# Kernel tuning notes

Hardware: AMD Instinct MI355X
Metric: run time of the kernel (lower is better)

The kernel has to match this reference:

```python
import jax, jax.numpy as jnp
import numpy as np

EPS = 1e-5

def layer_norm(x, w, b):
    mu = x.mean(-1, keepdims=True)
    var = x.var(-1, keepdims=True)
    return (x - mu) / jnp.sqrt(var + EPS) * w + b

def s5_forward(u, Lambda_re, Lambda_im, B_re, B_im, C_re, C_im, D, log_step):
    # u: [B, L, H]; diagonal S5 SSM with P complex states, ZOH discretization.
    Lam = (Lambda_re + 1j * Lambda_im).astype(jnp.complex64)          # [P]
    dt = jnp.exp(log_step).astype(jnp.complex64)                       # [P]
    Lam_bar = jnp.exp(Lam * dt)                                        # [P]
    Bc = (B_re + 1j * B_im).astype(jnp.complex64)                      # [P, H]
    B_bar = ((Lam_bar - 1.0) / Lam)[:, None] * Bc                      # [P, H]
    Bu = jnp.einsum('blh,ph->blp', u.astype(jnp.complex64), B_bar)     # [B, L, P]
    A = jnp.broadcast_to(Lam_bar, Bu.shape)                            # [B, L, P]

    def binop(e1, e2):
        a1, b1 = e1
        a2, b2 = e2
        return (a2 * a1, a2 * b1 + b2)

    _, xs = jax.lax.associative_scan(binop, (A, Bu), axis=1)           # [B, L, P]
    Cc = (C_re + 1j * C_im).astype(jnp.complex64)                      # [H, P]
    y = 2.0 * jnp.einsum('blp,hp->blh', xs, Cc).real + D * u           # [B, L, H]
    return y

def setup_inputs() -> dict:
    key = jax.random.key(0)
    ks = jax.random.split(key, 12)
    B, L, H, P = 4, 4096, 512, 512
    x = jax.random.normal(ks[0], (B, L, H), jnp.float32)
    # SSM params (HiPPO-like flavor: negative real part, spread imaginary part)
    Lambda_re = -(0.5 * jax.random.uniform(ks[1], (P,), jnp.float32) + 0.1)
    Lambda_im = jnp.pi * jnp.arange(P, dtype=jnp.float32)
    B_re = jax.random.normal(ks[2], (P, H), jnp.float32) / np.sqrt(2.0 * H)
    B_im = jax.random.normal(ks[3], (P, H), jnp.float32) / np.sqrt(2.0 * H)
    C_re = jax.random.normal(ks[4], (H, P), jnp.float32) / np.sqrt(P)
    C_im = jax.random.normal(ks[5], (H, P), jnp.float32) / np.sqrt(P)
    D = jax.random.normal(ks[6], (H,), jnp.float32)
    log_step = jax.random.uniform(ks[7], (P,), jnp.float32,
                                  minval=np.log(1e-3), maxval=np.log(1e-1))
    ln1_w = jnp.ones((H,), jnp.float32); ln1_b = jnp.zeros((H,), jnp.float32)
    ln2_w = jnp.ones((H,), jnp.float32); ln2_b = jnp.zeros((H,), jnp.float32)
    W_enc = jax.random.normal(ks[8], (2 * H, H), jnp.float32) / np.sqrt(H)
    W_dec = jax.random.normal(ks[9], (H, H), jnp.float32) / np.sqrt(H)
    return {"x": x, "ln1_w": ln1_w, "ln1_b": ln1_b,
            "Lambda_re": Lambda_re, "Lambda_im": Lambda_im,
            "B_re": B_re, "B_im": B_im, "C_re": C_re, "C_im": C_im,
            "D": D, "log_step": log_step,
            "ln2_w": ln2_w, "ln2_b": ln2_b, "W_enc": W_enc, "W_dec": W_dec}

def reference(x, ln1_w, ln1_b, Lambda_re, Lambda_im, B_re, B_im, C_re, C_im,
              D, log_step, ln2_w, ln2_b, W_enc, W_dec):
    fx = layer_norm(x, ln1_w, ln1_b)
    res = fx
    u = s5_forward(fx, Lambda_re, Lambda_im, B_re, B_im, C_re, C_im, D, log_step)
    h = jax.nn.gelu(u, approximate=False) + res  # eval mode: dropout = identity
    fx2 = layer_norm(h, ln2_w, ln2_b)
    e = fx2 @ W_enc.T                              # [B, L, 2H]
    a, g = jnp.split(e, 2, axis=-1)
    ff = a * jax.nn.gelu(g, approximate=False)     # GEGLU
    out = ff @ W_dec.T + fx2
    return out
```

## Files before the change

### kernel.cpp

```cpp
#include <hip/hip_runtime.h>
#include <math.h>

#define Bz 4
#define Lz 4096
#define Hz 512
#define Pz 512
#define Nz (Bz*Lz)
#define CL 32
#define NC (Lz/CL)
#define CS (Bz*NC*Pz)
#define EPSf 1e-5f

typedef unsigned short u16;
typedef unsigned int   u32;
typedef __attribute__((ext_vector_type(8))) short bf16x8;
typedef __attribute__((ext_vector_type(8))) short short8v;
typedef __attribute__((ext_vector_type(4))) float f32x4;

__device__ __forceinline__ float gelu_exact(float x){
    return 0.5f * x * (1.0f + erff(x * 0.70710678118654752f));
}
__device__ __forceinline__ u16 f2b(float f){
    union { float f; u32 u; } v; v.f = f;
    u32 u = v.u;
    u32 r = (u + 0x7FFFu + ((u >> 16) & 1u)) >> 16;
    return (u16)r;
}
__device__ __forceinline__ float b2f(u16 h){
    union { u32 u; float f; } v; v.u = ((u32)h) << 16; return v.f;
}

__device__ __forceinline__ void gload_lds16(const u16* g, u16* l){
    __builtin_amdgcn_global_load_lds(
        (const __attribute__((address_space(1))) void*)g,
        (__attribute__((address_space(3))) void*)l, 16, 0, 0);
}

__device__ __forceinline__ void load8(const float* p, float* v){
    f32x4 a = *(const f32x4*)p, c = *(const f32x4*)(p+4);
    #pragma unroll
    for (int j=0;j<4;++j){ v[j]=a[j]; v[4+j]=c[j]; }
}
__device__ __forceinline__ void load8(const u16* p, float* v){
    short8v s = *(const short8v*)p;
    #pragma unroll
    for (int j=0;j<8;++j) v[j] = b2f((u16)s[j]);
}

#define LN1B (Nz/4)
__global__ __launch_bounds__(256) void prep_kernel(
        const float* __restrict__ x,
        const float* __restrict__ ln1_w, const float* __restrict__ ln1_b,
        const float* __restrict__ B_re,  const float* __restrict__ B_im,
        const float* __restrict__ C_re,  const float* __restrict__ C_im,
        const float* __restrict__ W_enc, const float* __restrict__ W_dec,
        const float* __restrict__ Lre,   const float* __restrict__ Lim,
        const float* __restrict__ log_step,
        u16* __restrict__ fxb,
        u16* __restrict__ Bcat, u16* __restrict__ Ccat,
        u16* __restrict__ Wenc, u16* __restrict__ Wdec,
        float* __restrict__ prm){
    const int Q = 512*512;
    int blk = blockIdx.x;
    if (blk < LN1B){
        int row = blk*4 + (threadIdx.x >> 6);
        int l = threadIdx.x & 63;
        float v[8];
        load8(x + (size_t)row*Hz + l*8, v);
        float s = 0.f, q = 0.f;
        #pragma unroll
        for (int j=0;j<8;++j){ s += v[j]; q += v[j]*v[j]; }
        #pragma unroll
        for (int o=32;o;o>>=1){ s += __shfl_xor(s,o); q += __shfl_xor(q,o); }
        float mu = s * (1.0f/512.0f);
        float rs = rsqrtf(q * (1.0f/512.0f) - mu*mu + EPSf);
        short8v o8;
        #pragma unroll
        for (int j=0;j<8;++j){
            int m = l*8 + j;
            o8[j] = (short)f2b((v[j]-mu)*rs*ln1_w[m] + ln1_b[m]);
        }
        *(short8v*)&fxb[(size_t)row*Hz + l*8] = o8;
        return;
    }
    blk -= LN1B;
    if (blk >= 6*1024){
        int p = (blk - 6*1024)*256 + threadIdx.x;
        if (p >= Pz) return;
        float lr = Lre[p], li = Lim[p];
        float dt = expf(log_step[p]);
        float ar = lr*dt, ai = li*dt;
        float e = expf(ar);
        float Abr = e*cosf(ai), Abi = e*sinf(ai);
        prm[p]        = Abr;
        prm[Pz + p]   = Abi;
        float nr = Abr - 1.0f, ni = Abi;
        float d2 = lr*lr + li*li;
        prm[2*Pz + p] = (nr*lr + ni*li)/d2;
        prm[3*Pz + p] = (ni*lr - nr*li)/d2;
        float arC = ar*(float)CL, aiC = ai*(float)CL;
        float eC = expf(arC);
        prm[4*Pz + p] = eC*cosf(aiC);
        prm[5*Pz + p] = eC*sinf(aiC);
        return;
    }
    int i = blk*256 + threadIdx.x;
    if (i < Q){ int p=i>>9, h=i&511; Bcat[(size_t)(2*p)*512 + h]   = f2b(B_re[i]); return; }
    i -= Q;
    if (i < Q){ int p=i>>9, h=i&511; Bcat[(size_t)(2*p+1)*512 + h] = f2b(B_im[i]); return; }
    i -= Q;
    if (i < Q){
        int h = i >> 9, p = i & 511;
        Ccat[(size_t)h*1024 + 2*p]     = f2b(C_re[i]);
        Ccat[(size_t)h*1024 + 2*p + 1] = f2b(-C_im[i]);
        return;
    }
    i -= Q;
    if (i < 2*Q){ Wenc[i] = f2b(W_enc[i]); return; }
    i -= 2*Q;
    Wdec[i] = f2b(W_dec[i]);
}

template<typename T>
__global__ __launch_bounds__(256) void ln_kernel(const T* __restrict__ in,
                                                 const float* __restrict__ w,
                                                 const float* __restrict__ b,
                                                 u16* __restrict__ ob){
    int row = blockIdx.x*4 + (threadIdx.x >> 6);
    int l = threadIdx.x & 63;
    float v[8];
    load8(in + (size_t)row*Hz + l*8, v);
    float s = 0.f, q = 0.f;
    #pragma unroll
    for (int j=0;j<8;++j){ s += v[j]; q += v[j]*v[j]; }
    #pragma unroll
    for (int o=32;o;o>>=1){ s += __shfl_xor(s,o); q += __shfl_xor(q,o); }
    float mu = s * (1.0f/512.0f);
    float rs = rsqrtf(q * (1.0f/512.0f) - mu*mu + EPSf);
    short8v o8;
    #pragma unroll
    for (int j=0;j<8;++j){
        int m = l*8 + j;
        o8[j] = (short)f2b((v[j]-mu)*rs*w[m] + b[m]);
    }
    *(short8v*)&ob[(size_t)row*Hz + l*8] = o8;
}

#define EY    1
#define ERES  2
#define EGLU  3
#define ESCAN 4

#define ATW (256*64)
#define BTW (128*64)
#define TBW (ATW+BTW)

__device__ __forceinline__ void stageA256v(const u16* __restrict__ src, int ld,
                                           int row0, int kt, u16* lds){
    int lane = threadIdx.x & 63, w = threadIdx.x >> 6;
    #pragma unroll
    for (int q=0;q<4;++q){
        int c = w + q*8;
        int r = c*8 + (lane >> 3);
        int colE = 8*((lane & 7) ^ ((lane >> 3) & 7));
        gload_lds16(src + (size_t)(row0 + r)*ld + kt + colE, lds + c*512);
    }
}
__device__ __forceinline__ void stageB128v(const u16* __restrict__ src, int ld,
                                           int row0, int kt, u16* lds){
    int lane = threadIdx.x & 63, w = threadIdx.x >> 6;
    #pragma unroll
    for (int q=0;q<2;++q){
        int c = w + q*8;
        int r = c*8 + (lane >> 3);
        int colE = 8*((lane & 7) ^ ((lane >> 3) & 7));
        gload_lds16(src + (size_t)(row0 + r)*ld + kt + colE, lds + c*512);
    }
}
__device__ __forceinline__ void stageBglu(const u16* __restrict__ Wenc, int fb,
                                          int kt, u16* lds){
    int lane = threadIdx.x & 63, w = threadIdx.x >> 6;
    #pragma unroll
    for (int q=0;q<2;++q){
        int c = w + q*8;
        int v = c*8 + (lane >> 3);
        int vf = v >> 4, r = v & 15;
        int grow = ((vf & 1) ? 512 : 0) + fb + (vf >> 1)*16 + r;
        int colE = 8*((lane & 7) ^ ((lane >> 3) & 7));
        gload_lds16(Wenc + (size_t)grow*512 + kt + colE, lds + c*512);
    }
}

template<int K, int EPI>
__global__ __launch_bounds__(512)
void gemmv(const u16* __restrict__ A, const u16* __restrict__ Bw, int M,
           u16* __restrict__ outB,
           const u16* __restrict__ fxB,
           const float* __restrict__ Dv,
           const u16* __restrict__ resB,
           float* __restrict__ outF,
           const float* __restrict__ prm,
           float* __restrict__ ERe,
           float* __restrict__ EIm)
{
    constexpr int NT = K/64;
    constexpr int NP = (EPI==EGLU) ? 2 : 1;
    constexpr int TT = NT*NP;
    __shared__ u16 LDS[3*TBW];

    int nx = gridDim.x, ny = gridDim.y;
    int nwg = nx*ny;
    int lid = blockIdx.x + blockIdx.y*nx;
    int cpx = nwg >> 3;
    int gdx = (lid & 7)*cpx + (lid >> 3);
    int n0 = (gdx / ny) * 256 * NP;
    int mb = gdx % ny;
    int m0 = mb * 128;
    int fb = mb * 64;

    int l = threadIdx.x & 63;
    int w = threadIdx.x >> 6;
    int wm = w >> 1, wn = w & 1;
    int rb = wm*64, cb = wn*64;
    int lrow  = l & 15;
    int lcol0 = ((l >> 4)*8) ^ ((l & 7) << 3);
    int lcol1 = lcol0 ^ 32;
    int er = (l >> 4) * 4;
    int ec = l & 15;

    f32x4 acc[4][4];
    #pragma unroll
    for (int i=0;i<4;++i)
        #pragma unroll
        for (int j=0;j<4;++j) acc[i][j] = (f32x4)(0.f);

    stageA256v(A, K, n0, 0, &LDS[0]);
    if (EPI==EGLU) stageBglu(Bw, fb, 0, &LDS[ATW]); else stageB128v(Bw, K, m0, 0, &LDS[ATW]);
    stageA256v(A, K, n0, 64, &LDS[TBW]);
    if (EPI==EGLU) stageBglu(Bw, fb, 64, &LDS[TBW+ATW]); else stageB128v(Bw, K, m0, 64, &LDS[TBW+ATW]);

    for (int T=0; T<TT; ++T){
        if (T == TT-1){ asm volatile("s_waitcnt vmcnt(0)" ::: "memory"); }
        else          { asm volatile("s_waitcnt vmcnt(6)" ::: "memory"); }
        __builtin_amdgcn_s_barrier();
        if (T+2 < TT){
            u16* buf = &LDS[((T+2)%3)*TBW];
            int t2 = T+2;
            int ktn = (t2 % NT)*64;
            int rowA = n0 + (t2/NT)*256;
            stageA256v(A, K, rowA, ktn, buf);
            if (EPI==EGLU) stageBglu(Bw, fb, ktn, buf+ATW); else stageB128v(Bw, K, m0, ktn, buf+ATW);
        }
        const u16* Ab = &LDS[(T%3)*TBW];
        const u16* Bb = Ab + ATW;
        bf16x8 a0[4], a1[4], b0[4], b1[4];
        #pragma unroll
        for (int f=0; f<4; ++f){
            a0[f] = *(const bf16x8*)&Ab[(rb + f*16 + lrow)*64 + lcol0];
            a1[f] = *(const bf16x8*)&Ab[(rb + f*16 + lrow)*64 + lcol1];
        }
        #pragma unroll
        for (int g=0; g<4; ++g){
            b0[g] = *(const bf16x8*)&Bb[(cb + g*16 + lrow)*64 + lcol0];
            b1[g] = *(const bf16x8*)&Bb[(cb + g*16 + lrow)*64 + lcol1];
        }
        __builtin_amdgcn_s_setprio(1);
        #pragma unroll
        for (int f=0; f<4; ++f)
            #pragma unroll
            for (int g=0; g<4; ++g){
                acc[f][g] = __builtin_amdgcn_mfma_f32_16x16x32_bf16(a0[f], b0[g], acc[f][g], 0,0,0);
                acc[f][g] = __builtin_amdgcn_mfma_f32_16x16x32_bf16(a1[f], b1[g], acc[f][g], 0,0,0);
            }
        __builtin_amdgcn_s_setprio(0);
        if (EPI==EGLU && NP==2 && T == NT-1){
            #pragma unroll
            for (int fm=0; fm<4; ++fm)
                #pragma unroll
                for (int pr=0; pr<2; ++pr)
                    #pragma unroll
                    for (int q=0; q<4; ++q){
                        int n = n0 + rb + fm*16 + er + q;
                        int col = fb + (wn*2 + pr)*16 + ec;
                        float ffv = acc[fm][2*pr][q] * gelu_exact(acc[fm][2*pr+1][q]);
                        outB[(size_t)n*Hz + col] = f2b(ffv);
                    }
            #pragma unroll
            for (int i=0;i<4;++i)
                #pragma unroll
                for (int j=0;j<4;++j) acc[i][j] = (f32x4)(0.f);
        }
    }

    if (EPI == ESCAN){
        u16* gt = (u16*)LDS;
        __syncthreads();
        #pragma unroll
        for (int fm=0; fm<4; ++fm)
            #pragma unroll
            for (int g=0; g<4; ++g)
                #pragma unroll
                for (int q=0; q<4; ++q){
                    int rr = rb + fm*16 + er + q;
                    int cc = cb + g*16 + ec;
                    u16 hv = f2b(acc[fm][g][q]);
                    outB[(size_t)(n0 + rr)*M + (m0 + cc)] = hv;
                    gt[rr*128 + cc] = hv;
                }
        __syncthreads();
        int tid = threadIdx.x;
        int p = tid & 63, h = tid >> 6;
        int P = (m0 >> 1) + p;
        int b = n0 >> 12;
        int c = ((n0 & 4095) >> 5) + h;
        float Ar = prm[P], Ai = prm[Pz+P];
        float fre = prm[2*Pz+P], fim = prm[3*Pz+P];
        float xr = 0.f, xi = 0.f;
        int base = h*32*128 + 2*p;
        #pragma unroll 8
        for (int r = 0; r < 32; ++r){
            u32 v = *(const u32*)&gt[base + r*128];
            float gr = b2f((u16)(v & 0xffff));
            float gi = b2f((u16)(v >> 16));
            float br = fre*gr - fim*gi;
            float bi = fre*gi + fim*gr;
            float nr2 = Ar*xr - Ai*xi + br;
            float ni2 = Ar*xi + Ai*xr + bi;
            xr = nr2; xi = ni2;
        }
        size_t ci = ((size_t)(b*NC + c))*Pz + P;
        ERe[ci] = xr; EIm[ci] = xi;
    } else if (EPI == EGLU){
        int nb = n0 + (NP-1)*256;
        #pragma unroll
        for (int fm=0; fm<4; ++fm)
            #pragma unroll
            for (int pr=0; pr<2; ++pr)
                #pragma unroll
                for (int q=0; q<4; ++q){
                    int n = nb + rb + fm*16 + er + q;
                    int col = fb + (wn*2 + pr)*16 + ec;
                    float ffv = acc[fm][2*pr][q] * gelu_exact(acc[fm][2*pr+1][q]);
                    outB[(size_t)n*Hz + col] = f2b(ffv);
                }
    } else {
        #pragma unroll
        for (int fm=0; fm<4; ++fm)
            #pragma unroll
            for (int g=0; g<4; ++g)
                #pragma unroll
                for (int q=0; q<4; ++q){
                    int n = n0 + rb + fm*16 + er + q;
                    int m = m0 + cb + g*16 + ec;
                    float v = acc[fm][g][q];
                    if (EPI == EY){
                        size_t idx = (size_t)n*Hz + m;
                        float fxv = b2f(fxB[idx]);
                        float y = 2.0f*v + Dv[m]*fxv;
                        outB[idx] = f2b(gelu_exact(y) + fxv);
                    } else {
                        size_t idx = (size_t)n*Hz + m;
                        outF[idx] = v + b2f(resB[idx]);
                    }
                }
    }
}

__global__ __launch_bounds__(64) void scan_combine(const float* __restrict__ ERe,
                                                   const float* __restrict__ EIm,
                                                   const float* __restrict__ prm,
                                                   float* __restrict__ SinRe,
                                                   float* __restrict__ SinIm){
    int gt = blockIdx.x*64 + threadIdx.x;
    int b = gt / Pz, p = gt % Pz;
    float Ar = prm[4*Pz+p], Ai = prm[5*Pz+p];
    float Sr = 0.f, Si = 0.f;
    for (int c = 0; c < NC; ++c) {
        size_t idx = ((size_t)(b*NC + c))*Pz + p;
        SinRe[idx] = Sr; SinIm[idx] = Si;
        float er = ERe[idx], ei = EIm[idx];
        float nr = Ar*Sr - Ai*Si + er;
        float ni = Ar*Si + Ai*Sr + ei;
        Sr = nr; Si = ni;
    }
}

__global__ __launch_bounds__(64) void scan_phase2(u16* __restrict__ g,
                                                  const float* __restrict__ prm,
                                                  const float* __restrict__ SinRe,
                                                  const float* __restrict__ SinIm){
    int t = blockIdx.x;
    int ph = t & 1; t >>= 1;
    int c  = t % NC;
    int b  = t / NC;
    int p0 = ph*256 + threadIdx.x*4;
    int cbi = 2*p0;
    size_t base = ((size_t)(b*Lz + c*CL))*1024;
    size_t ci = ((size_t)(b*NC + c))*Pz + p0;
    float Ar[4], Ai[4], fr[4], fi[4], xr[4], xi[4];
    f32x4 sr4 = *(const f32x4*)&SinRe[ci];
    f32x4 si4 = *(const f32x4*)&SinIm[ci];
    #pragma unroll
    for (int j=0;j<4;++j){
        Ar[j]=prm[p0+j]; Ai[j]=prm[Pz+p0+j];
        fr[j]=prm[2*Pz+p0+j]; fi[j]=prm[3*Pz+p0+j];
        xr[j]=sr4[j]; xi[j]=si4[j];
    }
    for (int ll=0; ll<CL; ++ll){
        short8v v8 = *(const short8v*)&g[base + cbi];
        short8v o8;
        #pragma unroll
        for (int j=0;j<4;++j){
            float gr = b2f((u16)v8[2*j]), gi = b2f((u16)v8[2*j+1]);
            float br = fr[j]*gr - fi[j]*gi;
            float bi = fr[j]*gi + fi[j]*gr;
            float nr = Ar[j]*xr[j] - Ai[j]*xi[j] + br;
            float ni = Ar[j]*xi[j] + Ai[j]*xr[j] + bi;
            xr[j]=nr; xi[j]=ni;
            o8[2*j]   = (short)f2b(nr);
            o8[2*j+1] = (short)f2b(ni);
        }
        *(short8v*)&g[base + cbi] = o8;
        base += 1024;
    }
}

extern "C" void kernel_launch(void* const* d_in, const int* in_sizes, int n_in,
                              void* d_out, int out_size, void* d_ws, size_t ws_size,
                              hipStream_t stream) {
    const float* x        = (const float*)d_in[0];
    const float* ln1_w    = (const float*)d_in[1];
    const float* ln1_b    = (const float*)d_in[2];
    const float* Lre      = (const float*)d_in[3];
    const float* Lim      = (const float*)d_in[4];
    const float* B_re     = (const float*)d_in[5];
    const float* B_im     = (const float*)d_in[6];
    const float* C_re     = (const float*)d_in[7];
    const float* C_im     = (const float*)d_in[8];
    const float* Dv       = (const float*)d_in[9];
    const float* log_step = (const float*)d_in[10];
    const float* ln2_w    = (const float*)d_in[11];
    const float* ln2_b    = (const float*)d_in[12];
    const float* W_enc    = (const float*)d_in[13];
    const float* W_dec    = (const float*)d_in[14];
    float* out = (float*)d_out;

    const size_t NH = (size_t)Nz*Hz;
    char* W = (char*)d_ws;
    u16*   fxb  = (u16*)  (W);
    u16*   g    = (u16*)  (W + NH*2);
    u16*   hb   = (u16*)  (W + NH*6);
    u16*   fx2b = (u16*)  (W + NH*8);
    float* ERe  = (float*)(W + NH*10);
    float* EIm  = ERe + CS;
    float* SinRe= EIm + CS;
    float* SinIm= SinRe + CS;
    float* prm  = SinIm + CS;
    u16*   Bcat = (u16*)(prm + 6*Pz);
    u16*   Ccat = Bcat + 1024*512;
    u16*   Wenc = Ccat + 512*1024;
    u16*   Wdec = Wenc + 1024*512;

    prep_kernel<<<dim3(LN1B + 6*1024 + 2), dim3(256), 0, stream>>>(
        x, ln1_w, ln1_b, B_re, B_im, C_re, C_im, W_enc, W_dec,
        Lre, Lim, log_step, fxb, Bcat, Ccat, Wenc, Wdec, prm);

    gemmv<512,ESCAN><<<dim3(Nz/256, 1024/128), dim3(512), 0, stream>>>(
        fxb, Bcat, 1024, g, nullptr, nullptr, nullptr, nullptr, prm, ERe, EIm);

    scan_combine<<<dim3((Bz*Pz)/64), dim3(64), 0, stream>>>(ERe, EIm, prm, SinRe, SinIm);
    scan_phase2<<<dim3(Bz*NC*2), dim3(64), 0, stream>>>(g, prm, SinRe, SinIm);

    gemmv<1024,EY><<<dim3(Nz/256, 512/128), dim3(512), 0, stream>>>(
        g, Ccat, 512, hb, fxb, Dv, nullptr, nullptr, nullptr, nullptr, nullptr);

    ln_kernel<u16><<<dim3(Nz/4), dim3(256), 0, stream>>>(hb, ln2_w, ln2_b, fx2b);

    gemmv<512,EGLU><<<dim3(Nz/512, 1024/128), dim3(512), 0, stream>>>(
        fx2b, Wenc, 1024, fxb, nullptr, nullptr, nullptr, nullptr, nullptr, nullptr, nullptr);

    gemmv<512,ERES><<<dim3(Nz/256, 512/128), dim3(512), 0, stream>>>(
        fxb, Wdec, 512, nullptr, nullptr, nullptr, fx2b, out, nullptr, nullptr, nullptr);
}
```

Baseline: 163.7 us.

## Use dedicated 256x256 GEMM tile with K=32 stages for the B-projection scan kernel

```diff
diff --git a/kernel.cpp b/kernel.cpp
--- a/kernel.cpp
+++ b/kernel.cpp
@@ -149,7 +149,6 @@
 #define EY    1
 #define ERES  2
 #define EGLU  3
-#define ESCAN 4
 
 #define ATW (256*64)
 #define BTW (128*64)
@@ -198,10 +197,7 @@
            const u16* __restrict__ fxB,
            const float* __restrict__ Dv,
            const u16* __restrict__ resB,
-           float* __restrict__ outF,
-           const float* __restrict__ prm,
-           float* __restrict__ ERe,
-           float* __restrict__ EIm)
+           float* __restrict__ outF)
 {
     constexpr int NT = K/64;
     constexpr int NP = (EPI==EGLU) ? 2 : 1;
@@ -292,45 +288,7 @@
         }
     }
 
-    if (EPI == ESCAN){
-        u16* gt = (u16*)LDS;
-        __syncthreads();
-        #pragma unroll
-        for (int fm=0; fm<4; ++fm)
-            #pragma unroll
-            for (int g=0; g<4; ++g)
-                #pragma unroll
-                for (int q=0; q<4; ++q){
-                    int rr = rb + fm*16 + er + q;
-                    int cc = cb + g*16 + ec;
-                    u16 hv = f2b(acc[fm][g][q]);
-                    outB[(size_t)(n0 + rr)*M + (m0 + cc)] = hv;
-                    gt[rr*128 + cc] = hv;
-                }
-        __syncthreads();
-        int tid = threadIdx.x;
-        int p = tid & 63, h = tid >> 6;
-        int P = (m0 >> 1) + p;
-        int b = n0 >> 12;
-        int c = ((n0 & 4095) >> 5) + h;
-        float Ar = prm[P], Ai = prm[Pz+P];
-        float fre = prm[2*Pz+P], fim = prm[3*Pz+P];
-        float xr = 0.f, xi = 0.f;
-        int base = h*32*128 + 2*p;
-        #pragma unroll 8
-        for (int r = 0; r < 32; ++r){
-            u32 v = *(const u32*)&gt[base + r*128];
-            float gr = b2f((u16)(v & 0xffff));
-            float gi = b2f((u16)(v >> 16));
-            float br = fre*gr - fim*gi;
-            float bi = fre*gi + fim*gr;
-            float nr2 = Ar*xr - Ai*xi + br;
-            float ni2 = Ar*xi + Ai*xr + bi;
-            xr = nr2; xi = ni2;
-        }
-        size_t ci = ((size_t)(b*NC + c))*Pz + P;
-        ERe[ci] = xr; EIm[ci] = xi;
-    } else if (EPI == EGLU){
+    if (EPI == EGLU){
         int nb = n0 + (NP-1)*256;
         #pragma unroll
         for (int fm=0; fm<4; ++fm)
@@ -363,6 +321,145 @@
                         outF[idx] = v + b2f(resB[idx]);
                     }
                 }
+    }
+}
+
+#define ATW2 (256*32)
+#define BTW2 (128*32)
+#define TBW2 (ATW2 + 2*BTW2)
+
+__device__ __forceinline__ void stageA256k32(const u16* __restrict__ src,
+                                             int row0, int kt, u16* lds){
+    int lane = threadIdx.x & 63, w = threadIdx.x >> 6;
+    #pragma unroll
+    for (int q=0;q<2;++q){
+        int c = w + q*8;
+        int r = c*16 + (lane >> 2);
+        int colE = 8*((lane & 3) ^ ((lane >> 3) & 3));
+        gload_lds16(src + (size_t)(row0 + r)*512 + kt + colE, lds + c*512);
+    }
+}
+__device__ __forceinline__ void stageB128k32(const u16* __restrict__ src,
+                                             int row0, int kt, u16* lds){
+    int lane = threadIdx.x & 63, w = threadIdx.x >> 6;
+    int r = w*16 + (lane >> 2);
+    int colE = 8*((lane & 3) ^ ((lane >> 3) & 3));
+    gload_lds16(src + (size_t)(row0 + r)*512 + kt + colE, lds + w*512);
+}
+
+__global__ __launch_bounds__(512)
+void gemm1_scan2(const u16* __restrict__ A, const u16* __restrict__ Bw,
+                 u16* __restrict__ outB,
+                 const float* __restrict__ prm,
+                 float* __restrict__ ERe, float* __restrict__ EIm)
+{
+    constexpr int NT = 16;
+    __shared__ u16 LDS[3*TBW2];
+
+    int nwg = gridDim.x;
+    int lid = blockIdx.x;
+    int cpx = nwg >> 3;
+    int gdx = (lid & 7)*cpx + (lid >> 3);
+    int n0 = (gdx >> 2) * 256;
+    int mb = gdx & 3;
+    int m0a = mb*256, m0b = mb*256 + 128;
+
+    int l = threadIdx.x & 63;
+    int w = threadIdx.x >> 6;
+    int wm = w >> 1, wn = w & 1;
+    int rb = wm*64, cb = wn*64;
+    int lrow = l & 15;
+    int lcol = 8*((l >> 4) ^ ((l >> 1) & 3));
+    int er = (l >> 4) * 4;
+    int ec = l & 15;
+
+    f32x4 accA[4][4], accB[4][4];
+    #pragma unroll
+    for (int i=0;i<4;++i)
+        #pragma unroll
+        for (int j=0;j<4;++j){ accA[i][j]=(f32x4)(0.f); accB[i][j]=(f32x4)(0.f); }
+
+    stageA256k32(A, n0, 0, &LDS[0]);
+    stageB128k32(Bw, m0a, 0, &LDS[ATW2]);
+    stageB128k32(Bw, m0b, 0, &LDS[ATW2+BTW2]);
+    stageA256k32(A, n0, 32, &LDS[TBW2]);
+    stageB128k32(Bw, m0a, 32, &LDS[TBW2+ATW2]);
+    stageB128k32(Bw, m0b, 32, &LDS[TBW2+ATW2+BTW2]);
+
+    for (int T=0; T<NT; ++T){
+        if (T == NT-1){ asm volatile("s_waitcnt vmcnt(0)" ::: "memory"); }
+        else          { asm volatile("s_waitcnt vmcnt(4)" ::: "memory"); }
+        __builtin_amdgcn_s_barrier();
+        if (T+2 < NT){
+            u16* buf = &LDS[((T+2)%3)*TBW2];
+            int ktn = (T+2)*32;
+            stageA256k32(A, n0, ktn, buf);
+            stageB128k32(Bw, m0a, ktn, buf+ATW2);
+            stageB128k32(Bw, m0b, ktn, buf+ATW2+BTW2);
+        }
+        const u16* Ab = &LDS[(T%3)*TBW2];
+        const u16* B0 = Ab + ATW2;
+        const u16* B1 = B0 + BTW2;
+        bf16x8 af[4], b0[4], b1[4];
+        #pragma unroll
+        for (int f=0; f<4; ++f)
+            af[f] = *(const bf16x8*)&Ab[(rb + f*16 + lrow)*32 + lcol];
+        #pragma unroll
+        for (int g=0; g<4; ++g){
+            b0[g] = *(const bf16x8*)&B0[(cb + g*16 + lrow)*32 + lcol];
+            b1[g] = *(const bf16x8*)&B1[(cb + g*16 + lrow)*32 + lcol];
+        }
+        __builtin_amdgcn_s_setprio(1);
+        #pragma unroll
+        for (int f=0; f<4; ++f)
+            #pragma unroll
+            for (int g=0; g<4; ++g){
+                accA[f][g] = __builtin_amdgcn_mfma_f32_16x16x32_bf16(af[f], b0[g], accA[f][g], 0,0,0);
+                accB[f][g] = __builtin_amdgcn_mfma_f32_16x16x32_bf16(af[f], b1[g], accB[f][g], 0,0,0);
+            }
+        __builtin_amdgcn_s_setprio(0);
+    }
+
+    u16* gt = (u16*)LDS;
+    int b = n0 >> 12;
+    int tid = threadIdx.x;
+    #pragma unroll
+    for (int pan=0; pan<2; ++pan){
+        int m0p = pan ? m0b : m0a;
+        __syncthreads();
+        #pragma unroll
+        for (int fm=0; fm<4; ++fm)
+            #pragma unroll
+            for (int g=0; g<4; ++g)
+                #pragma unroll
+                for (int q=0; q<4; ++q){
+                    int rr = rb + fm*16 + er + q;
+                    int cc = cb + g*16 + ec;
+                    u16 hv = f2b(pan ? accB[fm][g][q] : accA[fm][g][q]);
+                    outB[(size_t)(n0 + rr)*1024 + (m0p + cc)] = hv;
+                    gt[rr*128 + cc] = hv;
+                }
+        __syncthreads();
+        int p = tid & 63, h = tid >> 6;
+        int P = (m0p >> 1) + p;
+        int c = ((n0 & 4095) >> 5) + h;
+        float Ar = prm[P], Ai = prm[Pz+P];
+        float fre = prm[2*Pz+P], fim = prm[3*Pz+P];
+        float xr = 0.f, xi = 0.f;
+        int base = h*32*128 + 2*p;
+        #pragma unroll 8
+        for (int r = 0; r < 32; ++r){
+            u32 v = *(const u32*)&gt[base + r*128];
+            float gr = b2f((u16)(v & 0xffff));
+            float gi = b2f((u16)(v >> 16));
+            float br = fre*gr - fim*gi;
+            float bi = fre*gi + fim*gr;
+            float nr2 = Ar*xr - Ai*xi + br;
+            float ni2 = Ar*xi + Ai*xr + bi;
+            xr = nr2; xi = ni2;
+        }
+        size_t ci = ((size_t)(b*NC + c))*Pz + P;
+        ERe[ci] = xr; EIm[ci] = xi;
     }
 }
 
@@ -465,20 +562,19 @@
         x, ln1_w, ln1_b, B_re, B_im, C_re, C_im, W_enc, W_dec,
         Lre, Lim, log_step, fxb, Bcat, Ccat, Wenc, Wdec, prm);
 
-    gemmv<512,ESCAN><<<dim3(Nz/256, 1024/128), dim3(512), 0, stream>>>(
-        fxb, Bcat, 1024, g, nullptr, nullptr, nullptr, nullptr, prm, ERe, EIm);
+    gemm1_scan2<<<dim3(256), dim3(512), 0, stream>>>(fxb, Bcat, g, prm, ERe, EIm);
 
     scan_combine<<<dim3((Bz*Pz)/64), dim3(64), 0, stream>>>(ERe, EIm, prm, SinRe, SinIm);
     scan_phase2<<<dim3(Bz*NC*2), dim3(64), 0, stream>>>(g, prm, SinRe, SinIm);
 
     gemmv<1024,EY><<<dim3(Nz/256, 512/128), dim3(512), 0, stream>>>(
-        g, Ccat, 512, hb, fxb, Dv, nullptr, nullptr, nullptr, nullptr, nullptr);
+        g, Ccat, 512, hb, fxb, Dv, nullptr, nullptr);
 
     ln_kernel<u16><<<dim3(Nz/4), dim3(256), 0, stream>>>(hb, ln2_w, ln2_b, fx2b);
 
     gemmv<512,EGLU><<<dim3(Nz/512, 1024/128), dim3(512), 0, stream>>>(
-        fx2b, Wenc, 1024, fxb, nullptr, nullptr, nullptr, nullptr, nullptr, nullptr, nullptr);
+        fx2b, Wenc, 1024, fxb, nullptr, nullptr, nullptr, nullptr);
 
     gemmv<512,ERES><<<dim3(Nz/256, 512/128), dim3(512), 0, stream>>>(
-        fxb, Wdec, 512, nullptr, nullptr, nullptr, fx2b, out, nullptr, nullptr, nullptr);
-}
+        fxb, Wdec, 512, nullptr, nullptr, nullptr, fx2b, out);
+}
```

After: 161.5 us, median of 2. About the same (-1.3%).
